# Kernel optimization log

Measured on AMD Instinct MI355X. Metric: run time of the kernel, lower is better.

Reference implementation:

```python
import jax, jax.numpy as jnp
import numpy as np

V, E, B, T = 50000, 512, 8, 512

def setup_inputs() -> dict:
    key = jax.random.key(0)
    ks = jax.random.split(key, 9)
    s_ih = 1.0 / np.sqrt(E)
    return {
        "x": jax.random.randint(ks[0], (B, T), 0, V, dtype=jnp.int64),
        "y": jax.random.randint(ks[1], (B, T), 0, V, dtype=jnp.int64),
        "embedding": jax.random.normal(ks[2], (V, E), dtype=jnp.float32),
        "w_ih": jax.random.uniform(ks[3], (4 * E, E), jnp.float32, -s_ih, s_ih),
        "w_hh": jax.random.uniform(ks[4], (4 * E, E), jnp.float32, -s_ih, s_ih),
        "b_ih": jax.random.uniform(ks[5], (4 * E,), jnp.float32, -s_ih, s_ih),
        "b_hh": jax.random.uniform(ks[6], (4 * E,), jnp.float32, -s_ih, s_ih),
        "dec_w": jax.random.uniform(ks[7], (V, E), jnp.float32, -s_ih, s_ih),
        "dec_b": jax.random.uniform(ks[8], (V,), jnp.float32, -s_ih, s_ih),
    }

def _lstm(embed, w_ih, w_hh, b_ih, b_hh):
    # embed: [B, T, E]. Precompute input projections for all timesteps.
    xproj = jnp.einsum("bte,ge->btg", embed, w_ih) + b_ih  # [B, T, 4E]
    xproj = jnp.swapaxes(xproj, 0, 1)                      # [T, B, 4E]
    h0 = jnp.zeros((embed.shape[0], w_hh.shape[1]), embed.dtype)
    c0 = jnp.zeros_like(h0)

    def step(carry, xp_t):
        h, c = carry
        gates = xp_t + h @ w_hh.T + b_hh          # [B, 4E]
        i, f, g, o = jnp.split(gates, 4, axis=-1)  # PyTorch gate order: i,f,g,o
        i = jax.nn.sigmoid(i)
        f = jax.nn.sigmoid(f)
        g = jnp.tanh(g)
        o = jax.nn.sigmoid(o)
        c = f * c + i * g
        h = o * jnp.tanh(c)
        return (h, c), h

    _, hs = jax.lax.scan(step, (h0, c0), xproj)   # hs: [T, B, E]
    return jnp.swapaxes(hs, 0, 1)                 # [B, T, E]

def reference(x, y, embedding, w_ih, w_hh, b_ih, b_hh, dec_w, dec_b):
    embed = embedding[x]                                   # [B, T, E]
    lstm_out = _lstm(embed, w_ih, w_hh, b_ih, b_hh)        # [B, T, E]
    y_pred = jnp.einsum("bte,ve->btv", lstm_out, dec_w) + dec_b  # [B, T, V]
    return y_pred
```

## Files before the change

### kernel.cpp

```cpp
#include <hip/hip_runtime.h>
#include <hip/hip_bf16.h>
#include <stdint.h>

typedef short bf16x8 __attribute__((ext_vector_type(8)));
typedef float f32x4 __attribute__((ext_vector_type(4)));

typedef const __attribute__((address_space(1))) unsigned int glob_u32;
typedef __attribute__((address_space(3))) unsigned int lds_u32;

__device__ __forceinline__ void gl_lds16(const void* g, void* s) {
  __builtin_amdgcn_global_load_lds((glob_u32*)g, (lds_u32*)s, 16, 0, 0);
}

__device__ __forceinline__ unsigned short f2bf(float f) {
  __hip_bfloat16 h = __float2bfloat16(f);
  return __builtin_bit_cast(unsigned short, h);
}
__device__ __forceinline__ float bf2f(unsigned short u) {
  __hip_bfloat16 h = __builtin_bit_cast(__hip_bfloat16, u);
  return __bfloat162float(h);
}

__device__ __forceinline__ float sigm_fast(float x) {
  float e = __expf(-x);
  return __builtin_amdgcn_rcpf(1.f + e);
}
__device__ __forceinline__ float tanh_fast(float x) {
  float e = __expf(2.f * x);
  return 1.f - 2.f * __builtin_amdgcn_rcpf(e + 1.f);
}

__device__ __forceinline__ float readl(float v, int lane) {
  return __builtin_bit_cast(float,
      __builtin_amdgcn_readlane(__builtin_bit_cast(int, v), lane));
}

__global__ void split_hl(const float* __restrict__ src,
                         unsigned short* __restrict__ hi,
                         unsigned short* __restrict__ lo, int n4) {
  int i = blockIdx.x * blockDim.x + threadIdx.x;
  if (i >= n4) return;
  float4 v = reinterpret_cast<const float4*>(src)[i];
  ushort4 h, l;
  h.x = f2bf(v.x); l.x = f2bf(v.x - bf2f(h.x));
  h.y = f2bf(v.y); l.y = f2bf(v.y - bf2f(h.y));
  h.z = f2bf(v.z); l.z = f2bf(v.z - bf2f(h.z));
  h.w = f2bf(v.w); l.w = f2bf(v.w - bf2f(h.w));
  reinterpret_cast<ushort4*>(hi)[i] = h;
  reinterpret_cast<ushort4*>(lo)[i] = l;
}

__global__ void split_h(const float* __restrict__ src,
                        unsigned short* __restrict__ hi, int n4) {
  int i = blockIdx.x * blockDim.x + threadIdx.x;
  if (i >= n4) return;
  float4 v = reinterpret_cast<const float4*>(src)[i];
  ushort4 h;
  h.x = f2bf(v.x); h.y = f2bf(v.y); h.z = f2bf(v.z); h.w = f2bf(v.w);
  reinterpret_cast<ushort4*>(hi)[i] = h;
}

__global__ void gather_split(const int* __restrict__ x, const float* __restrict__ emb,
                             unsigned short* __restrict__ hi,
                             unsigned short* __restrict__ lo) {
  int i = blockIdx.x * 256 + threadIdx.x;
  int m = i >> 7, k4 = i & 127;
  long row = x[m];
  float4 v = reinterpret_cast<const float4*>(emb + row * 512)[k4];
  ushort4 h, l;
  h.x = f2bf(v.x); l.x = f2bf(v.x - bf2f(h.x));
  h.y = f2bf(v.y); l.y = f2bf(v.y - bf2f(h.y));
  h.z = f2bf(v.z); l.z = f2bf(v.z - bf2f(h.z));
  h.w = f2bf(v.w); l.w = f2bf(v.w - bf2f(h.w));
  reinterpret_cast<ushort4*>(hi)[m * 128 + k4] = h;
  reinterpret_cast<ushort4*>(lo)[m * 128 + k4] = l;
}

__global__ __launch_bounds__(256) void gemm_split(
    const unsigned short* __restrict__ Ahi, const unsigned short* __restrict__ Alo,
    const unsigned short* __restrict__ Bhi, const unsigned short* __restrict__ Blo,
    float* __restrict__ C, const float* __restrict__ bias1,
    const float* __restrict__ bias2, int N, int mtiles) {
  __shared__ unsigned short lds[4][128 * 64];
  int nwg = gridDim.x;
  int wid = (blockIdx.x & 7) * (nwg >> 3) + (blockIdx.x >> 3);
  int mt = wid % mtiles, nt = wid / mtiles;
  int m0 = mt * 128, n0 = nt * 128;
  int tid = threadIdx.x, l = tid & 63, w = tid >> 6;
  int wm = (w & 1) * 64, wn = (w >> 1) * 64;

  f32x4 acc[4][4];
#pragma unroll
  for (int a = 0; a < 4; ++a)
#pragma unroll
    for (int b = 0; b < 4; ++b) acc[a][b] = f32x4{0.f, 0.f, 0.f, 0.f};

  const unsigned short* srcs[4] = {Ahi, Alo, Bhi, Blo};

  for (int kc = 0; kc < 8; ++kc) {
    __syncthreads();
#pragma unroll
    for (int tile = 0; tile < 4; ++tile) {
      const unsigned short* src = srcs[tile];
      int rbase = (tile < 2) ? m0 : n0;
#pragma unroll
      for (int i = 0; i < 4; ++i) {
        int G = (i * 4 + w) * 64 + l;
        int r = G >> 3, g = G & 7;
        int row = rbase + r;
        long gb = (long)row * 1024 + kc * 128 + ((g * 16) ^ ((r & 7) << 4));
        gl_lds16((const char*)src + gb, (char*)(&lds[tile][0]) + (i * 4 + w) * 1024);
      }
    }
    __syncthreads();

    const char* ldsb = (const char*)&lds[0][0];
#pragma unroll
    for (int ks = 0; ks < 2; ++ks) {
      bf16x8 ah[4], al[4], bh[4], bl[4];
      int biw = ks * 64 + ((l >> 4) * 16);
#pragma unroll
      for (int fm = 0; fm < 4; ++fm) {
        int row = wm + fm * 16 + (l & 15);
        int off = row * 128 + (biw ^ ((row & 7) << 4));
        ah[fm] = *reinterpret_cast<const bf16x8*>(ldsb + off);
        al[fm] = *reinterpret_cast<const bf16x8*>(ldsb + 16384 + off);
      }
#pragma unroll
      for (int fn = 0; fn < 4; ++fn) {
        int row = wn + fn * 16 + (l & 15);
        int off = row * 128 + (biw ^ ((row & 7) << 4));
        bh[fn] = *reinterpret_cast<const bf16x8*>(ldsb + 32768 + off);
        bl[fn] = *reinterpret_cast<const bf16x8*>(ldsb + 49152 + off);
      }
#pragma unroll
      for (int fm = 0; fm < 4; ++fm)
#pragma unroll
        for (int fn = 0; fn < 4; ++fn) {
          acc[fm][fn] = __builtin_amdgcn_mfma_f32_16x16x32_bf16(ah[fm], bh[fn], acc[fm][fn], 0, 0, 0);
          acc[fm][fn] = __builtin_amdgcn_mfma_f32_16x16x32_bf16(ah[fm], bl[fn], acc[fm][fn], 0, 0, 0);
          acc[fm][fn] = __builtin_amdgcn_mfma_f32_16x16x32_bf16(al[fm], bh[fn], acc[fm][fn], 0, 0, 0);
        }
    }
  }

#pragma unroll
  for (int fn = 0; fn < 4; ++fn) {
    int n = n0 + wn + fn * 16 + (l & 15);
    float bs = bias1[n];
    if (bias2) bs += bias2[n];
#pragma unroll
    for (int fm = 0; fm < 4; ++fm) {
      int mb = m0 + wm + fm * 16 + (l >> 4) * 4;
#pragma unroll
      for (int j = 0; j < 4; ++j)
        C[(long)(mb + j) * N + n] = acc[fm][fn][j] + bs;
    }
  }
}

__global__ __launch_bounds__(256) void gemm_plain(
    const unsigned short* __restrict__ Ahi, const unsigned short* __restrict__ Bhi,
    float* __restrict__ C, const float* __restrict__ bias1, int N) {
  __shared__ unsigned short lds[2][128 * 64];
  int xcd = blockIdx.x & 7;
  int wid = blockIdx.x >> 3;
  int mt = xcd * 4 + (wid & 3);
  int nt = wid >> 2;
  int m0 = mt * 128, n0 = nt * 128;
  int tid = threadIdx.x, l = tid & 63, w = tid >> 6;
  int wm = (w & 1) * 64, wn = (w >> 1) * 64;

  f32x4 acc[4][4];
#pragma unroll
  for (int a = 0; a < 4; ++a)
#pragma unroll
    for (int b = 0; b < 4; ++b) acc[a][b] = f32x4{0.f, 0.f, 0.f, 0.f};

  const unsigned short* srcs[2] = {Ahi, Bhi};

  for (int kc = 0; kc < 8; ++kc) {
    __syncthreads();
#pragma unroll
    for (int tile = 0; tile < 2; ++tile) {
      const unsigned short* src = srcs[tile];
      int rbase = (tile < 1) ? m0 : n0;
#pragma unroll
      for (int i = 0; i < 4; ++i) {
        int G = (i * 4 + w) * 64 + l;
        int r = G >> 3, g = G & 7;
        int row = rbase + r;
        if (tile == 1 && row >= N) row = n0;
        long gb = (long)row * 1024 + kc * 128 + ((g * 16) ^ ((r & 7) << 4));
        gl_lds16((const char*)src + gb, (char*)(&lds[tile][0]) + (i * 4 + w) * 1024);
      }
    }
    __syncthreads();

    const char* ldsb = (const char*)&lds[0][0];
#pragma unroll
    for (int ks = 0; ks < 2; ++ks) {
      bf16x8 ah[4], bh[4];
      int biw = ks * 64 + ((l >> 4) * 16);
#pragma unroll
      for (int fm = 0; fm < 4; ++fm) {
        int row = wm + fm * 16 + (l & 15);
        int off = row * 128 + (biw ^ ((row & 7) << 4));
        ah[fm] = *reinterpret_cast<const bf16x8*>(ldsb + off);
      }
#pragma unroll
      for (int fn = 0; fn < 4; ++fn) {
        int row = wn + fn * 16 + (l & 15);
        int off = row * 128 + (biw ^ ((row & 7) << 4));
        bh[fn] = *reinterpret_cast<const bf16x8*>(ldsb + 16384 + off);
      }
#pragma unroll
      for (int fm = 0; fm < 4; ++fm)
#pragma unroll
        for (int fn = 0; fn < 4; ++fn)
          acc[fm][fn] = __builtin_amdgcn_mfma_f32_16x16x32_bf16(ah[fm], bh[fn], acc[fm][fn], 0, 0, 0);
    }
  }

#pragma unroll
  for (int fn = 0; fn < 4; ++fn) {
    int n = n0 + wn + fn * 16 + (l & 15);
    if (n < N) {
      float bs = bias1[n];
#pragma unroll
      for (int fm = 0; fm < 4; ++fm) {
        int mb = m0 + wm + fm * 16 + (l >> 4) * 4;
#pragma unroll
        for (int j = 0; j < 4; ++j)
          C[(long)(mb + j) * N + n] = acc[fm][fn][j] + bs;
      }
    }
  }
}

__global__ __launch_bounds__(256, 1) void lstm_persistent(
    const float* __restrict__ xproj,
    const float* __restrict__ whh,
    float* lstm_f32,
    unsigned short* __restrict__ lstm_hi) {
  int bid = blockIdx.x;
  int batch = bid & 7, slice = bid >> 3;
  int tid = threadIdx.x, l = tid & 63, w = tid >> 6;
  int g = l >> 4, e = l & 15;
  long R = (long)g * 512 + slice * 16 + e;

  __shared__ float part_s[2][4][64];

  float wr[128];
  {
    const float4* wp = reinterpret_cast<const float4*>(whh + R * 512 + w * 128);
#pragma unroll
    for (int jj = 0; jj < 32; ++jj) {
      float4 v = wp[jj];
      wr[jj * 4 + 0] = v.x; wr[jj * 4 + 1] = v.y;
      wr[jj * 4 + 2] = v.z; wr[jj * 4 + 3] = v.w;
    }
  }
#pragma unroll
  for (int jj = 0; jj < 128; jj += 4)
    asm volatile("" : "+v"(wr[jj]), "+v"(wr[jj + 1]), "+v"(wr[jj + 2]), "+v"(wr[jj + 3]));

  const float* xbase = xproj + (long)batch * 512 * 2048 + g * 512 + slice * 16 + e;
  float* hrow_base = lstm_f32 + (long)batch * 512 * 512;
  float c_reg = 0.f;

  float xp_cur = 0.f, xp_nxt = 0.f;
  if (w == 0) xp_cur = xbase[0];

  for (int t = 0; t < 512; ++t) {
    if (w == 0 && t < 511) xp_nxt = xbase[(long)(t + 1) * 2048];

    float a0 = 0.f, a1 = 0.f, a2 = 0.f, a3 = 0.f;
    if (t > 0) {
      const unsigned long long* src = reinterpret_cast<const unsigned long long*>(
          hrow_base + (long)(t - 1) * 512 + w * 128) + l;
#define PLOAD() __hip_atomic_load(src, __ATOMIC_RELAXED, __HIP_MEMORY_SCOPE_AGENT)
      unsigned long long p0 = PLOAD(), p1 = PLOAD(), p2 = PLOAD(), p3 = PLOAD();
      while ((unsigned)p0 == 0xFFFFFFFFu || (unsigned)(p0 >> 32) == 0xFFFFFFFFu) {
        p0 = p1; p1 = p2; p2 = p3; p3 = PLOAD();
      }
#undef PLOAD
      float hlo = __builtin_bit_cast(float, (unsigned)p0);
      float hhi = __builtin_bit_cast(float, (unsigned)(p0 >> 32));
#pragma unroll
      for (int j = 0; j < 64; ++j) {
        float hx = readl(hlo, j);
        float hy = readl(hhi, j);
        a0 = fmaf(wr[2 * j], hx, a0);
        a1 = fmaf(wr[2 * j + 1], hy, a1);
      }
    }
    part_s[t & 1][w][l] = a0 + a1 + (a2 + a3);
    __syncthreads();

    if (w == 0) {
      float sum = xp_cur + (part_s[t & 1][0][l] + part_s[t & 1][1][l]) +
                  (part_s[t & 1][2][l] + part_s[t & 1][3][l]);
      float val = (g == 2) ? tanh_fast(sum) : sigm_fast(sum);
      float vf = __shfl(val, e + 16);
      float vg = __shfl(val, e + 32);
      float vo = __shfl(val, e + 48);
      if (l < 16) {
        float c = vf * c_reg + val * vg;
        c_reg = c;
        float h = vo * tanh_fast(c);
        long oidx = ((long)batch * 512 + t) * 512 + slice * 16 + l;
        __hip_atomic_store(reinterpret_cast<unsigned int*>(lstm_f32) + oidx,
                           __builtin_bit_cast(unsigned int, h),
                           __ATOMIC_RELAXED, __HIP_MEMORY_SCOPE_AGENT);
        lstm_hi[oidx] = f2bf(h);
      }
      xp_cur = xp_nxt;
    }
  }
}

extern "C" void kernel_launch(void* const* d_in, const int* in_sizes, int n_in,
                              void* d_out, int out_size, void* d_ws, size_t ws_size,
                              hipStream_t stream) {
  const int*   x         = (const int*)d_in[0];
  const float* embedding = (const float*)d_in[2];
  const float* w_ih      = (const float*)d_in[3];
  const float* w_hh      = (const float*)d_in[4];
  const float* b_ih      = (const float*)d_in[5];
  const float* b_hh      = (const float*)d_in[6];
  const float* dec_w     = (const float*)d_in[7];
  const float* dec_b     = (const float*)d_in[8];

  char* ws = (char*)d_ws;
  float* xproj = (float*)ws;                      ws += (size_t)4096 * 2048 * 4;
  float* lstmf = (float*)ws;                      ws += (size_t)4096 * 512 * 4;
  unsigned short* lstm_hi = (unsigned short*)ws;  ws += (size_t)4096 * 512 * 2;
  unsigned short* emb_hi  = (unsigned short*)ws;  ws += (size_t)4096 * 512 * 2;
  unsigned short* emb_lo  = (unsigned short*)ws;  ws += (size_t)4096 * 512 * 2;
  unsigned short* wih_hi  = (unsigned short*)ws;  ws += (size_t)2048 * 512 * 2;
  unsigned short* wih_lo  = (unsigned short*)ws;  ws += (size_t)2048 * 512 * 2;
  unsigned short* dw_hi   = (unsigned short*)ws;  ws += (size_t)50000 * 512 * 2;

  hipMemsetAsync(lstmf, 0xFF, (size_t)4096 * 512 * 4, stream);

  split_hl<<<1024, 256, 0, stream>>>(w_ih, wih_hi, wih_lo, 2048 * 512 / 4);
  split_h<<<25000, 256, 0, stream>>>(dec_w, dw_hi, 50000 * 512 / 4);
  gather_split<<<2048, 256, 0, stream>>>(x, embedding, emb_hi, emb_lo);

  gemm_split<<<32 * 16, 256, 0, stream>>>(emb_hi, emb_lo, wih_hi, wih_lo, xproj,
                                          b_ih, b_hh, 2048, 32);

  {
    void* args[] = {(void*)&xproj, (void*)&w_hh, (void*)&lstmf, (void*)&lstm_hi};
    hipLaunchCooperativeKernel((void*)lstm_persistent, dim3(256), dim3(256), args, 0, stream);
  }

  gemm_plain<<<32 * 391, 256, 0, stream>>>(lstm_hi, dw_hi, (float*)d_out, dec_b, 50000);
}
```

Measured before the change: 1.458 ms.

## Interleave four batches per LSTM block to hide cross-block h latency

Each persistent block now handles four batch rows in round-robin instead of one, so the grid drops from 256 to 64 blocks. While one batch's matvec runs, the block prefetches the next batch's hidden-state row, which hides the polling latency of the global-memory handoff between blocks. The trade-off is that each block does four times the serial work per timestep on fewer CUs. The __syncthreads call is replaced by an explicit lgkmcnt wait plus s_barrier.

```diff
diff --git a/kernel.cpp b/kernel.cpp
--- a/kernel.cpp
+++ b/kernel.cpp
@@ -244,7 +244,7 @@
     float* lstm_f32,
     unsigned short* __restrict__ lstm_hi) {
   int bid = blockIdx.x;
-  int batch = bid & 7, slice = bid >> 3;
+  int slice = bid & 31, bgrp = bid >> 5;
   int tid = threadIdx.x, l = tid & 63, w = tid >> 6;
   int g = l >> 4, e = l & 15;
   long R = (long)g * 512 + slice * 16 + e;
@@ -265,57 +265,76 @@
   for (int jj = 0; jj < 128; jj += 4)
     asm volatile("" : "+v"(wr[jj]), "+v"(wr[jj + 1]), "+v"(wr[jj + 2]), "+v"(wr[jj + 3]));
 
-  const float* xbase = xproj + (long)batch * 512 * 2048 + g * 512 + slice * 16 + e;
-  float* hrow_base = lstm_f32 + (long)batch * 512 * 512;
-  float c_reg = 0.f;
-
-  float xp_cur = 0.f, xp_nxt = 0.f;
-  if (w == 0) xp_cur = xbase[0];
+  const float* xbase[4];
+  const unsigned long long* hbase[4];
+#pragma unroll
+  for (int ib = 0; ib < 4; ++ib) {
+    int b = bgrp * 4 + ib;
+    xbase[ib] = xproj + (long)b * 512 * 2048 + g * 512 + slice * 16 + e;
+    hbase[ib] = reinterpret_cast<const unsigned long long*>(
+        lstm_f32 + (long)b * 512 * 512);
+  }
+
+  float c_reg[4] = {0.f, 0.f, 0.f, 0.f};
+  float xp_cur[4], xp_nxt[4] = {0.f, 0.f, 0.f, 0.f};
+#pragma unroll
+  for (int ib = 0; ib < 4; ++ib)
+    if (w == 0) xp_cur[ib] = xbase[ib][0];
+
+  unsigned long long pend = 0;
 
   for (int t = 0; t < 512; ++t) {
-    if (w == 0 && t < 511) xp_nxt = xbase[(long)(t + 1) * 2048];
-
-    float a0 = 0.f, a1 = 0.f, a2 = 0.f, a3 = 0.f;
-    if (t > 0) {
-      const unsigned long long* src = reinterpret_cast<const unsigned long long*>(
-          hrow_base + (long)(t - 1) * 512 + w * 128) + l;
-#define PLOAD() __hip_atomic_load(src, __ATOMIC_RELAXED, __HIP_MEMORY_SCOPE_AGENT)
-      unsigned long long p0 = PLOAD(), p1 = PLOAD(), p2 = PLOAD(), p3 = PLOAD();
-      while ((unsigned)p0 == 0xFFFFFFFFu || (unsigned)(p0 >> 32) == 0xFFFFFFFFu) {
-        p0 = p1; p1 = p2; p2 = p3; p3 = PLOAD();
-      }
-#undef PLOAD
-      float hlo = __builtin_bit_cast(float, (unsigned)p0);
-      float hhi = __builtin_bit_cast(float, (unsigned)(p0 >> 32));
-#pragma unroll
-      for (int j = 0; j < 64; ++j) {
-        float hx = readl(hlo, j);
-        float hy = readl(hhi, j);
-        a0 = fmaf(wr[2 * j], hx, a0);
-        a1 = fmaf(wr[2 * j + 1], hy, a1);
-      }
-    }
-    part_s[t & 1][w][l] = a0 + a1 + (a2 + a3);
-    __syncthreads();
-
-    if (w == 0) {
-      float sum = xp_cur + (part_s[t & 1][0][l] + part_s[t & 1][1][l]) +
-                  (part_s[t & 1][2][l] + part_s[t & 1][3][l]);
-      float val = (g == 2) ? tanh_fast(sum) : sigm_fast(sum);
-      float vf = __shfl(val, e + 16);
-      float vg = __shfl(val, e + 32);
-      float vo = __shfl(val, e + 48);
-      if (l < 16) {
-        float c = vf * c_reg + val * vg;
-        c_reg = c;
-        float h = vo * tanh_fast(c);
-        long oidx = ((long)batch * 512 + t) * 512 + slice * 16 + l;
-        __hip_atomic_store(reinterpret_cast<unsigned int*>(lstm_f32) + oidx,
-                           __builtin_bit_cast(unsigned int, h),
-                           __ATOMIC_RELAXED, __HIP_MEMORY_SCOPE_AGENT);
-        lstm_hi[oidx] = f2bf(h);
-      }
-      xp_cur = xp_nxt;
+#pragma unroll
+    for (int ib = 0; ib < 4; ++ib) {
+      unsigned long long cur = pend;
+      {
+        bool do_issue = (ib == 3) ? (t < 511) : (t > 0);
+        long row = (ib == 3) ? t : (t - 1);
+        if (do_issue)
+          pend = __hip_atomic_load(hbase[(ib + 1) & 3] + row * 256 + w * 64 + l,
+                                   __ATOMIC_RELAXED, __HIP_MEMORY_SCOPE_AGENT);
+      }
+      if (w == 0 && t < 511) xp_nxt[ib] = xbase[ib][(long)(t + 1) * 2048];
+
+      float a0 = 0.f, a1 = 0.f;
+      if (t > 0) {
+        while ((unsigned)cur == 0xFFFFFFFFu || (unsigned)(cur >> 32) == 0xFFFFFFFFu)
+          cur = __hip_atomic_load(hbase[ib] + (long)(t - 1) * 256 + w * 64 + l,
+                                  __ATOMIC_RELAXED, __HIP_MEMORY_SCOPE_AGENT);
+        float hlo = __builtin_bit_cast(float, (unsigned)cur);
+        float hhi = __builtin_bit_cast(float, (unsigned)(cur >> 32));
+#pragma unroll
+        for (int j = 0; j < 64; ++j) {
+          float hx = readl(hlo, j);
+          float hy = readl(hhi, j);
+          a0 = fmaf(wr[2 * j], hx, a0);
+          a1 = fmaf(wr[2 * j + 1], hy, a1);
+        }
+      }
+      part_s[ib & 1][w][l] = a0 + a1;
+      asm volatile("s_waitcnt lgkmcnt(0)" ::: "memory");
+      __builtin_amdgcn_s_barrier();
+      asm volatile("s_waitcnt lgkmcnt(0)" ::: "memory");
+
+      if (w == 0) {
+        float sum = xp_cur[ib] + (part_s[ib & 1][0][l] + part_s[ib & 1][1][l]) +
+                    (part_s[ib & 1][2][l] + part_s[ib & 1][3][l]);
+        float val = (g == 2) ? tanh_fast(sum) : sigm_fast(sum);
+        float vf = __shfl(val, e + 16);
+        float vg = __shfl(val, e + 32);
+        float vo = __shfl(val, e + 48);
+        if (l < 16) {
+          float c = vf * c_reg[ib] + val * vg;
+          c_reg[ib] = c;
+          float h = vo * tanh_fast(c);
+          long oidx = (((long)(bgrp * 4 + ib) * 512 + t) * 512) + slice * 16 + l;
+          __hip_atomic_store(reinterpret_cast<unsigned int*>(lstm_f32) + oidx,
+                             __builtin_bit_cast(unsigned int, h),
+                             __ATOMIC_RELAXED, __HIP_MEMORY_SCOPE_AGENT);
+          lstm_hi[oidx] = f2bf(h);
+        }
+        xp_cur[ib] = xp_nxt[ib];
+      }
     }
   }
 }
@@ -353,7 +372,7 @@
 
   {
     void* args[] = {(void*)&xproj, (void*)&w_hh, (void*)&lstmf, (void*)&lstm_hi};
-    hipLaunchCooperativeKernel((void*)lstm_persistent, dim3(256), dim3(256), args, 0, stream);
+    hipLaunchCooperativeKernel((void*)lstm_persistent, dim3(64), dim3(256), args, 0, stream);
   }
 
   gemm_plain<<<32 * 391, 256, 0, stream>>>(lstm_hi, dw_hi, (float*)d_out, dec_b, 50000);
```

Result: slower. 2.547 ms (+74.7%).

## Split LSTM recurrence rows across waves with DPP reductions, drop block barrier

Applied to the files above, without the earlier changes.

The persistent LSTM kernel now gives each wave four complete hidden units (all four gates) and splits the K dimension across lanes. Each wave reduces its 16 dot products with DPP wave sums, so the shared-memory partial sums and the per-step __syncthreads are gone, and every wave computes its own gate activations and cell update. This removes the cross-wave barrier and the 128 serialized readlane broadcasts from each step. In exchange it adds 16 DPP reduction chains per step, and every lane now polls and loads 8 h values, which raises the polling traffic on the global h buffer.

```diff
diff --git a/kernel.cpp b/kernel.cpp
--- a/kernel.cpp
+++ b/kernel.cpp
@@ -30,9 +30,24 @@
   return 1.f - 2.f * __builtin_amdgcn_rcpf(e + 1.f);
 }
 
-__device__ __forceinline__ float readl(float v, int lane) {
-  return __builtin_bit_cast(float,
-      __builtin_amdgcn_readlane(__builtin_bit_cast(int, v), lane));
+template <int CTRL, int RM>
+__device__ __forceinline__ float dpp_add(float s) {
+  int v = __builtin_amdgcn_update_dpp(0, __builtin_bit_cast(int, s), CTRL, RM, 0xf, true);
+  return s + __builtin_bit_cast(float, v);
+}
+template <int CTRL>
+__device__ __forceinline__ float dpp_mov(float s) {
+  int v = __builtin_amdgcn_update_dpp(0, __builtin_bit_cast(int, s), CTRL, 0xf, 0xf, true);
+  return __builtin_bit_cast(float, v);
+}
+__device__ __forceinline__ float wave_sum(float s) {
+  s = dpp_add<0x111, 0xf>(s);
+  s = dpp_add<0x112, 0xf>(s);
+  s = dpp_add<0x114, 0xf>(s);
+  s = dpp_add<0x118, 0xf>(s);
+  s = dpp_add<0x142, 0xa>(s);
+  s = dpp_add<0x143, 0xc>(s);
+  return s;
 }
 
 __global__ void split_hl(const float* __restrict__ src,
@@ -246,78 +261,95 @@
   int bid = blockIdx.x;
   int batch = bid & 7, slice = bid >> 3;
   int tid = threadIdx.x, l = tid & 63, w = tid >> 6;
-  int g = l >> 4, e = l & 15;
-  long R = (long)g * 512 + slice * 16 + e;
-
-  __shared__ float part_s[2][4][64];
 
   float wr[128];
-  {
-    const float4* wp = reinterpret_cast<const float4*>(whh + R * 512 + w * 128);
-#pragma unroll
-    for (int jj = 0; jj < 32; ++jj) {
-      float4 v = wp[jj];
-      wr[jj * 4 + 0] = v.x; wr[jj * 4 + 1] = v.y;
-      wr[jj * 4 + 2] = v.z; wr[jj * 4 + 3] = v.w;
-    }
+#pragma unroll
+  for (int r2 = 0; r2 < 16; ++r2) {
+    long Rr = (long)(r2 & 3) * 512 + slice * 16 + w * 4 + (r2 >> 2);
+    const float4* wp = reinterpret_cast<const float4*>(whh + Rr * 512 + 8 * l);
+    float4 v0 = wp[0], v1 = wp[1];
+    wr[r2 * 8 + 0] = v0.x; wr[r2 * 8 + 1] = v0.y;
+    wr[r2 * 8 + 2] = v0.z; wr[r2 * 8 + 3] = v0.w;
+    wr[r2 * 8 + 4] = v1.x; wr[r2 * 8 + 5] = v1.y;
+    wr[r2 * 8 + 6] = v1.z; wr[r2 * 8 + 7] = v1.w;
   }
 #pragma unroll
   for (int jj = 0; jj < 128; jj += 4)
     asm volatile("" : "+v"(wr[jj]), "+v"(wr[jj + 1]), "+v"(wr[jj + 2]), "+v"(wr[jj + 3]));
 
-  const float* xbase = xproj + (long)batch * 512 * 2048 + g * 512 + slice * 16 + e;
-  float* hrow_base = lstm_f32 + (long)batch * 512 * 512;
+  const float* xbase = nullptr;
+  float xp_cur = 0.f, xp_nxt = 0.f;
+  if (l < 16) {
+    long Rx = (long)(l & 3) * 512 + slice * 16 + w * 4 + (l >> 2);
+    xbase = xproj + (long)batch * 512 * 2048 + Rx;
+    xp_cur = xbase[0];
+  }
+
+  float* hbuf = lstm_f32 + (long)batch * 512 * 512;
+  int eg = slice * 16 + w * 4 + (l >> 2);
   float c_reg = 0.f;
 
-  float xp_cur = 0.f, xp_nxt = 0.f;
-  if (w == 0) xp_cur = xbase[0];
+#define AL(p) __hip_atomic_load((p), __ATOMIC_RELAXED, __HIP_MEMORY_SCOPE_AGENT)
+#define BAD(u) (((unsigned)(u)) == 0xFFFFFFFFu || ((unsigned)((u) >> 32)) == 0xFFFFFFFFu)
 
   for (int t = 0; t < 512; ++t) {
-    if (w == 0 && t < 511) xp_nxt = xbase[(long)(t + 1) * 2048];
-
-    float a0 = 0.f, a1 = 0.f, a2 = 0.f, a3 = 0.f;
+    if (l < 16 && t < 511) xp_nxt = xbase[(long)(t + 1) * 2048];
+
+    float vS = 0.f;
     if (t > 0) {
-      const unsigned long long* src = reinterpret_cast<const unsigned long long*>(
-          hrow_base + (long)(t - 1) * 512 + w * 128) + l;
-#define PLOAD() __hip_atomic_load(src, __ATOMIC_RELAXED, __HIP_MEMORY_SCOPE_AGENT)
-      unsigned long long p0 = PLOAD(), p1 = PLOAD(), p2 = PLOAD(), p3 = PLOAD();
-      while ((unsigned)p0 == 0xFFFFFFFFu || (unsigned)(p0 >> 32) == 0xFFFFFFFFu) {
-        p0 = p1; p1 = p2; p2 = p3; p3 = PLOAD();
-      }
-#undef PLOAD
-      float hlo = __builtin_bit_cast(float, (unsigned)p0);
-      float hhi = __builtin_bit_cast(float, (unsigned)(p0 >> 32));
-#pragma unroll
-      for (int j = 0; j < 64; ++j) {
-        float hx = readl(hlo, j);
-        float hy = readl(hhi, j);
-        a0 = fmaf(wr[2 * j], hx, a0);
-        a1 = fmaf(wr[2 * j + 1], hy, a1);
-      }
-    }
-    part_s[t & 1][w][l] = a0 + a1 + (a2 + a3);
-    __syncthreads();
-
-    if (w == 0) {
-      float sum = xp_cur + (part_s[t & 1][0][l] + part_s[t & 1][1][l]) +
-                  (part_s[t & 1][2][l] + part_s[t & 1][3][l]);
-      float val = (g == 2) ? tanh_fast(sum) : sigm_fast(sum);
-      float vf = __shfl(val, e + 16);
-      float vg = __shfl(val, e + 32);
-      float vo = __shfl(val, e + 48);
-      if (l < 16) {
-        float c = vf * c_reg + val * vg;
-        c_reg = c;
-        float h = vo * tanh_fast(c);
-        long oidx = ((long)batch * 512 + t) * 512 + slice * 16 + l;
-        __hip_atomic_store(reinterpret_cast<unsigned int*>(lstm_f32) + oidx,
-                           __builtin_bit_cast(unsigned int, h),
-                           __ATOMIC_RELAXED, __HIP_MEMORY_SCOPE_AGENT);
-        lstm_hi[oidx] = f2bf(h);
-      }
-      xp_cur = xp_nxt;
-    }
-  }
+      const unsigned long long* hp =
+          reinterpret_cast<const unsigned long long*>(hbuf + (long)(t - 1) * 512) + 4 * l;
+      unsigned long long A0 = AL(hp), A1 = AL(hp + 1), A2 = AL(hp + 2), A3 = AL(hp + 3);
+      unsigned long long B0 = AL(hp), B1 = AL(hp + 1), B2 = AL(hp + 2), B3 = AL(hp + 3);
+      unsigned long long C0 = AL(hp), C1 = AL(hp + 1), C2 = AL(hp + 2), C3 = AL(hp + 3);
+      while (BAD(A0) || BAD(A1) || BAD(A2) || BAD(A3)) {
+        A0 = B0; A1 = B1; A2 = B2; A3 = B3;
+        B0 = C0; B1 = C1; B2 = C2; B3 = C3;
+        C0 = AL(hp); C1 = AL(hp + 1); C2 = AL(hp + 2); C3 = AL(hp + 3);
+      }
+      float hv[8];
+      hv[0] = __builtin_bit_cast(float, (unsigned)A0);
+      hv[1] = __builtin_bit_cast(float, (unsigned)(A0 >> 32));
+      hv[2] = __builtin_bit_cast(float, (unsigned)A1);
+      hv[3] = __builtin_bit_cast(float, (unsigned)(A1 >> 32));
+      hv[4] = __builtin_bit_cast(float, (unsigned)A2);
+      hv[5] = __builtin_bit_cast(float, (unsigned)(A2 >> 32));
+      hv[6] = __builtin_bit_cast(float, (unsigned)A3);
+      hv[7] = __builtin_bit_cast(float, (unsigned)(A3 >> 32));
+
+#pragma unroll
+      for (int r2 = 0; r2 < 16; ++r2) {
+        float a = 0.f;
+#pragma unroll
+        for (int j = 0; j < 8; ++j) a = fmaf(wr[r2 * 8 + j], hv[j], a);
+        float s = wave_sum(a);
+        int tot = __builtin_amdgcn_readlane(__builtin_bit_cast(int, s), 63);
+        float totf = __builtin_bit_cast(float, tot);
+        vS = (l == r2) ? totf : vS;
+      }
+    }
+
+    float sum = vS + xp_cur;
+    bool isg = (l & 3) == 2;
+    float sg = sigm_fast(isg ? 2.f * sum : sum);
+    float val = isg ? 2.f * sg - 1.f : sg;
+    float v1 = dpp_mov<0xB1>(val);
+    float v2 = dpp_mov<0x4E>(val);
+    float v3 = dpp_mov<0x1B>(val);
+    if (l < 16 && (l & 3) == 0) {
+      float c = v1 * c_reg + val * v2;
+      c_reg = c;
+      float h = v3 * tanh_fast(c);
+      long oidx = ((long)batch * 512 + t) * 512 + eg;
+      __hip_atomic_store(reinterpret_cast<unsigned int*>(lstm_f32) + oidx,
+                         __builtin_bit_cast(unsigned int, h),
+                         __ATOMIC_RELAXED, __HIP_MEMORY_SCOPE_AGENT);
+      lstm_hi[oidx] = f2bf(h);
+    }
+    xp_cur = xp_nxt;
+  }
+#undef AL
+#undef BAD
 }
 
 extern "C" void kernel_launch(void* const* d_in, const int* in_sizes, int n_in,
```

Result: slower. 3.925 ms (+169.2%).
